# Performance work log

Hardware: AMD Instinct MI355X
Metric: run time of the kernel (lower is better)

Reference implementation:

```python
import jax, jax.numpy as jnp
import numpy as np

EPS = 1e-12  # torch f.normalize eps


def _rms_norm(x, g):
    # f.normalize(x, dim=1) * g * sqrt(C): L2-normalize over channel dim
    c = x.shape[1]
    n = jnp.maximum(jnp.linalg.norm(x, axis=1, keepdims=True), EPS)
    return x / n * g * (c ** 0.5)


def setup_inputs() -> dict:
    key = jax.random.key(0)
    ks = jax.random.split(key, 5)
    b, dim, H, W = 32, 256, 64, 64
    heads, dim_head, num_mem = 4, 32, 4
    hidden = heads * dim_head
    return {
        "x": jax.random.normal(ks[0], (b, dim, H, W), dtype=jnp.float32),
        "g1": jnp.ones((1, dim, 1, 1), dtype=jnp.float32),
        "mem_kv": jax.random.normal(ks[1], (2, heads, dim_head, num_mem), dtype=jnp.float32),
        "w_qkv": jax.random.normal(ks[2], (3 * hidden, dim), dtype=jnp.float32) * (1.0 / np.sqrt(dim)),
        "w_out": jax.random.normal(ks[3], (dim, hidden), dtype=jnp.float32) * (1.0 / np.sqrt(hidden)),
        "b_out": jnp.zeros((dim,), dtype=jnp.float32),
        "g2": jnp.ones((1, dim, 1, 1), dtype=jnp.float32),
    }


def reference(x, g1, mem_kv, w_qkv, w_out, b_out, g2):
    b, c, H, W = x.shape
    _, heads, dim_head, num_mem = mem_kv.shape
    n = H * W
    scale = dim_head ** -0.5

    xn = _rms_norm(x, g1)
    # 1x1 conv qkv projection: [b, 3*hidden, H, W]
    qkv = jnp.einsum('oc,bchw->bohw', w_qkv, xn)
    hidden = heads * dim_head
    q, k, v = jnp.split(qkv, 3, axis=1)
    # b (h d) x y -> b h d (x y)
    q = q.reshape(b, heads, dim_head, n)
    k = k.reshape(b, heads, dim_head, n)
    v = v.reshape(b, heads, dim_head, n)

    mk = jnp.broadcast_to(mem_kv[0], (b, heads, dim_head, num_mem))
    mv = jnp.broadcast_to(mem_kv[1], (b, heads, dim_head, num_mem))
    k = jnp.concatenate([mk, k], axis=-1)
    v = jnp.concatenate([mv, v], axis=-1)

    q = jax.nn.softmax(q, axis=-2) * scale  # softmax over head dim d
    k = jax.nn.softmax(k, axis=-1)          # softmax over sequence n

    context = jnp.einsum('bhdn,bhen->bhde', k, v)   # [b,h,d,e]
    out = jnp.einsum('bhde,bhdn->bhen', context, q)  # [b,h,e,n]
    out = out.reshape(b, hidden, H, W)

    o = jnp.einsum('oc,bchw->bohw', w_out, out) + b_out[None, :, None, None]
    return _rms_norm(o, g2)
```

## Files before the change

kernel.cpp:

```cpp
#include <hip/hip_runtime.h>
#include <math.h>

#define CC   256
#define HW   4096
#define OC3  384
#define HID  128
#define DH   32
#define NM   4
#define NPART 8
#define SCALE 0.17677669529663688f

typedef __bf16 bf16x8 __attribute__((ext_vector_type(8)));
typedef float  f32x4  __attribute__((ext_vector_type(4)));

__device__ __forceinline__ ushort f2bf(float x) {
    union { float f; unsigned u; } v; v.f = x;
    unsigned r = v.u + 0x7fffu + ((v.u >> 16) & 1u);
    return (ushort)(r >> 16);
}
__device__ __forceinline__ float bf2f(ushort b) {
    union { unsigned u; float f; } v; v.u = ((unsigned)b) << 16; return v.f;
}
__device__ __forceinline__ void g2l16(const void* g, void* l) {
    __builtin_amdgcn_global_load_lds(
        (const __attribute__((address_space(1))) void*)g,
        (__attribute__((address_space(3))) void*)l, 16, 0, 0);
}

__global__ void k_prep(const float* __restrict__ wqkv, const float* __restrict__ g1,
                       const float* __restrict__ wout,
                       ushort* __restrict__ wq2t, ushort* __restrict__ woutt) {
    int o = blockIdx.x, t = threadIdx.x;
    wq2t[(size_t)o * CC + t] = f2bf(wqkv[(size_t)o * CC + t] * g1[t] * 16.0f);
    if (o < CC && t < HID) woutt[(size_t)o * HID + t] = f2bf(wout[(size_t)o * HID + t]);
}

__global__ __launch_bounds__(256) void k_xn(const float* __restrict__ x,
                                            ushort* __restrict__ xnT) {
    __shared__ float xt[256 * 36];
    __shared__ float ps[8 * 33];
    __shared__ float invn[32];
    int tid = threadIdx.x;
    int pix0 = blockIdx.x * 32;
    int b = pix0 >> 12, hw0 = pix0 & 4095;
    int p = tid & 31, cg = tid >> 5;
    const float* xb = x + (size_t)b * CC * HW + hw0;
    {
        int cr = tid >> 3;
        int chunk = tid & 7;
        #pragma unroll
        for (int pass = 0; pass < 8; ++pass) {
            int c = pass * 32 + cr;
            float4 v = *(const float4*)&xb[(size_t)c * HW + chunk * 4];
            *(float4*)&xt[c * 36 + chunk * 4] = v;
        }
    }
    __syncthreads();
    float s = 0.f;
    #pragma unroll 8
    for (int i = 0; i < 32; ++i) { float v = xt[(cg * 32 + i) * 36 + p]; s += v * v; }
    ps[cg * 33 + p] = s;
    __syncthreads();
    if (tid < 32) {
        float t = 0.f;
        #pragma unroll
        for (int g = 0; g < 8; ++g) t += ps[g * 33 + tid];
        invn[tid] = 1.0f / fmaxf(sqrtf(t), 1e-12f);
    }
    __syncthreads();
    float inv = invn[p];
    ushort* dst = xnT + ((size_t)(pix0 + p)) * CC + cg * 32;
    #pragma unroll
    for (int q = 0; q < 4; ++q) {
        uint4 pk; ushort* o8 = (ushort*)&pk;
        #pragma unroll
        for (int i = 0; i < 8; ++i) o8[i] = f2bf(xt[(cg * 32 + q * 8 + i) * 36 + p] * inv);
        *(uint4*)&dst[q * 8] = pk;
    }
}

__global__ __launch_bounds__(256) void k_qkv(const ushort* __restrict__ wq2t,
        const ushort* __restrict__ xnT, ushort* __restrict__ qkv) {
    __shared__ ushort As[128 * 32];
    __shared__ ushort Bs[128 * 32];
    int tid = threadIdx.x;
    int lin = blockIdx.x + 3 * (blockIdx.y + 32 * blockIdx.z);
    int swz = (lin & 7) * 384 + (lin >> 3);
    int m0 = (swz % 3) * 128;
    int t_ = swz / 3;
    int p0 = (t_ & 31) * 128;
    int b  = t_ >> 5;
    int lane = tid & 63, wid = tid >> 6;
    int l15 = tid & 15, quad = (tid >> 4) & 3;
    int wm = wid >> 1, wn = wid & 1;
    int rsub = lane >> 2, csub = (lane & 3) * 8;
    const ushort* Ab = wq2t + (size_t)m0 * CC;
    const ushort* Bb = xnT + ((size_t)(b * HW + p0)) * CC;
    f32x4 acc[4][4];
    #pragma unroll
    for (int i = 0; i < 4; ++i)
        #pragma unroll
        for (int j = 0; j < 4; ++j) acc[i][j] = (f32x4){0.f, 0.f, 0.f, 0.f};
    for (int k0 = 0; k0 < CC; k0 += 32) {
        __syncthreads();
        #pragma unroll
        for (int q = 0; q < 2; ++q) {
            int rw = wid * 32 + q * 16;
            g2l16(Ab + (size_t)(rw + rsub) * CC + k0 + csub, &As[rw * 32]);
            g2l16(Bb + (size_t)(rw + rsub) * CC + k0 + csub, &Bs[rw * 32]);
        }
        __syncthreads();
        bf16x8 af[4], bfr[4];
        #pragma unroll
        for (int mt = 0; mt < 4; ++mt)
            af[mt] = *(const bf16x8*)&As[(wm * 64 + mt * 16 + l15) * 32 + quad * 8];
        #pragma unroll
        for (int nt = 0; nt < 4; ++nt)
            bfr[nt] = *(const bf16x8*)&Bs[(wn * 64 + nt * 16 + l15) * 32 + quad * 8];
        #pragma unroll
        for (int mt = 0; mt < 4; ++mt)
            #pragma unroll
            for (int nt = 0; nt < 4; ++nt)
                acc[mt][nt] = __builtin_amdgcn_mfma_f32_16x16x32_bf16(
                                  af[mt], bfr[nt], acc[mt][nt], 0, 0, 0);
    }
    #pragma unroll
    for (int mt = 0; mt < 4; ++mt) {
        int o = m0 + wm * 64 + mt * 16 + quad * 4;
        #pragma unroll
        for (int nt = 0; nt < 4; ++nt) {
            int pix = p0 + wn * 64 + nt * 16 + l15;
            ushort* dst = qkv + ((size_t)(b * OC3 + o)) * HW + pix;
            #pragma unroll
            for (int r = 0; r < 4; ++r) dst[(size_t)r * HW] = f2bf(acc[mt][nt][r]);
        }
    }
}

__global__ void k_ksoft(const ushort* __restrict__ qkv, const float* __restrict__ memkv,
                        float* __restrict__ kmaxb, float* __restrict__ rsumb) {
    int row = blockIdx.x * 4 + (threadIdx.x >> 6);
    int lane = threadIdx.x & 63;
    int b = row >> 7, hd = row & 127;
    const ushort* kp = qkv + ((size_t)(b * OC3 + HID + hd)) * HW;
    float m = -1e30f;
    #pragma unroll
    for (int i0 = 0; i0 < HW; i0 += 512) {
        uint4 pk = *(const uint4*)&kp[i0 + lane * 8];
        const ushort* e = (const ushort*)&pk;
        #pragma unroll
        for (int j = 0; j < 8; ++j) m = fmaxf(m, bf2f(e[j]));
    }
    #pragma unroll
    for (int s = 1; s < 64; s <<= 1) m = fmaxf(m, __shfl_xor(m, s));
    const float* mk = memkv + hd * NM;
    #pragma unroll
    for (int j = 0; j < NM; ++j) m = fmaxf(m, mk[j]);
    float s = 0.f;
    #pragma unroll
    for (int i0 = 0; i0 < HW; i0 += 512) {
        uint4 pk = *(const uint4*)&kp[i0 + lane * 8];
        const ushort* e = (const ushort*)&pk;
        #pragma unroll
        for (int j = 0; j < 8; ++j) s += __expf(bf2f(e[j]) - m);
    }
    #pragma unroll
    for (int t = 1; t < 64; t <<= 1) s += __shfl_xor(s, t);
    #pragma unroll
    for (int j = 0; j < NM; ++j) s += __expf(mk[j] - m);
    if (lane == 0) { kmaxb[row] = m; rsumb[row] = 1.0f / s; }
}

__global__ __launch_bounds__(256) void k_ctx(const ushort* __restrict__ qkv,
        const float* __restrict__ memkv, const float* __restrict__ kmaxb,
        const float* __restrict__ rsumb, float* __restrict__ ctxp) {
    __shared__ float kl[DH][65];
    __shared__ float vl[DH][65];
    __shared__ float red[256 * 33];
    int tid = threadIdx.x;
    int bh = blockIdx.x;
    int part = blockIdx.y;
    int b = bh >> 2, h = bh & 3;
    int lr = tid >> 3;
    int nn8 = (tid & 7) * 8;
    const ushort* kp = qkv + ((size_t)(b * OC3 + HID + h * DH) + lr) * HW + part * 512 + nn8;
    const ushort* vp = qkv + ((size_t)(b * OC3 + 2 * HID + h * DH) + lr) * HW + part * 512 + nn8;
    int rowbase = bh * DH;
    float kmr = kmaxb[rowbase + lr], rsr = rsumb[rowbase + lr];
    int slot = tid & 31, nng = tid >> 5;
    int d0 = (slot >> 2) * 4, e0 = (slot & 3) * 8;
    float acc[4][8];
    #pragma unroll
    for (int i = 0; i < 4; ++i)
        #pragma unroll
        for (int j = 0; j < 8; ++j) acc[i][j] = 0.f;
    for (int n0 = 0; n0 < 512; n0 += 64) {
        __syncthreads();
        uint4 kv4 = *(const uint4*)&kp[n0];
        uint4 vv4 = *(const uint4*)&vp[n0];
        const ushort* ke = (const ushort*)&kv4;
        const ushort* ve = (const ushort*)&vv4;
        #pragma unroll
        for (int j = 0; j < 8; ++j) {
            kl[lr][nn8 + j] = __expf(bf2f(ke[j]) - kmr) * rsr;
            vl[lr][nn8 + j] = bf2f(ve[j]);
        }
        __syncthreads();
        #pragma unroll 2
        for (int t = 0; t < 8; ++t) {
            int nn = nng * 8 + t;
            float kv[4], vv[8];
            #pragma unroll
            for (int i = 0; i < 4; ++i) kv[i] = kl[d0 + i][nn];
            #pragma unroll
            for (int j = 0; j < 8; ++j) vv[j] = vl[e0 + j][nn];
            #pragma unroll
            for (int i = 0; i < 4; ++i)
                #pragma unroll
                for (int j = 0; j < 8; ++j) acc[i][j] += kv[i] * vv[j];
        }
    }
    __syncthreads();
    #pragma unroll
    for (int i = 0; i < 4; ++i)
        #pragma unroll
        for (int j = 0; j < 8; ++j) red[tid * 33 + i * 8 + j] = acc[i][j];
    __syncthreads();
    #pragma unroll
    for (int q = 0; q < 4; ++q) {
        int o = tid * 4 + q;
        int d = o >> 5, e = o & 31;
        int sl = (d >> 2) * 4 + (e >> 3);
        int k = (d & 3) * 8 + (e & 7);
        float s = 0.f;
        #pragma unroll
        for (int g = 0; g < 8; ++g) s += red[(g * 32 + sl) * 33 + k];
        if (part == 0) {
            float km = kmaxb[rowbase + d], rsm = rsumb[rowbase + d];
            #pragma unroll
            for (int m = 0; m < NM; ++m) {
                float kw = __expf(memkv[(h * DH + d) * NM + m] - km) * rsm;
                s += kw * memkv[512 + (h * DH + e) * NM + m];
            }
        }
        ctxp[(size_t)part * 131072 + (size_t)bh * 1024 + o] = s;
    }
}

__global__ __launch_bounds__(256) void k_w2(const float* __restrict__ ctxp,
        const ushort* __restrict__ woutt, ushort* __restrict__ W2) {
    __shared__ ushort ctxb[4 * 32 * 40];
    int tid = threadIdx.x, b = blockIdx.x;
    int wid = tid >> 6;
    int l15 = tid & 15, quad = (tid >> 4) & 3;
    #pragma unroll
    for (int j = 0; j < 16; ++j) {
        int idx = tid + j * 256;
        float s = 0.f;
        #pragma unroll
        for (int p = 0; p < NPART; ++p)
            s += ctxp[(size_t)p * 131072 + (size_t)b * 4096 + idx];
        int h = idx >> 10, d = (idx >> 5) & 31, e = idx & 31;
        ctxb[(h * 32 + d) * 40 + e] = f2bf(s);
    }
    __syncthreads();
    #pragma unroll
    for (int h = 0; h < 4; ++h) {
        f32x4 acc[4][2];
        #pragma unroll
        for (int i = 0; i < 4; ++i)
            #pragma unroll
            for (int j = 0; j < 2; ++j) acc[i][j] = (f32x4){0.f, 0.f, 0.f, 0.f};
        bf16x8 af[4], bfr[2];
        #pragma unroll
        for (int mt = 0; mt < 4; ++mt)
            af[mt] = *(const bf16x8*)&woutt[(size_t)(wid * 64 + mt * 16 + l15) * HID
                                            + h * DH + quad * 8];
        #pragma unroll
        for (int nt = 0; nt < 2; ++nt)
            bfr[nt] = *(const bf16x8*)&ctxb[(h * 32 + nt * 16 + l15) * 40 + quad * 8];
        #pragma unroll
        for (int mt = 0; mt < 4; ++mt)
            #pragma unroll
            for (int nt = 0; nt < 2; ++nt)
                acc[mt][nt] = __builtin_amdgcn_mfma_f32_16x16x32_bf16(
                                  af[mt], bfr[nt], acc[mt][nt], 0, 0, 0);
        #pragma unroll
        for (int mt = 0; mt < 4; ++mt)
            #pragma unroll
            for (int nt = 0; nt < 2; ++nt)
                #pragma unroll
                for (int r = 0; r < 4; ++r) {
                    int oc = wid * 64 + mt * 16 + quad * 4 + r;
                    int d  = nt * 16 + l15;
                    W2[((size_t)b * CC + oc) * HID + h * DH + d] = f2bf(acc[mt][nt][r]);
                }
    }
}

__global__ __launch_bounds__(256) void k_final(const ushort* __restrict__ qkv,
        const ushort* __restrict__ W2, const float* __restrict__ bout,
        const float* __restrict__ g2, float* __restrict__ y) {
    __shared__ __align__(16) ushort sq[64 * 136];
    __shared__ __align__(16) ushort Ws[256 * 32];
    __shared__ float red[64 * 17];
    __shared__ float invs[64];
    __shared__ float bl[256];
    __shared__ float gl[256];
    int tid = threadIdx.x;
    int b = blockIdx.y;
    int hwb = blockIdx.x * 64;
    int lane = tid & 63, wid = tid >> 6;
    int l15 = tid & 15, quad = (tid >> 4) & 3;
    bl[tid] = bout[tid];
    gl[tid] = g2[tid];

    {
        const ushort* qp = qkv + ((size_t)b * OC3 + wid * DH) * HW + hwb + lane;
        float vd[32];
        float m = -1e30f;
        #pragma unroll
        for (int d = 0; d < 32; ++d) {
            float v = bf2f(qp[(size_t)d * HW]);
            vd[d] = v; m = fmaxf(m, v);
        }
        float s = 0.f;
        #pragma unroll
        for (int d = 0; d < 32; ++d) { float e = __expf(vd[d] - m); vd[d] = e; s += e; }
        float r_ = SCALE / s;
        #pragma unroll
        for (int q8 = 0; q8 < 4; ++q8) {
            uint4 pk; ushort* o8 = (ushort*)&pk;
            #pragma unroll
            for (int i = 0; i < 8; ++i) o8[i] = f2bf(vd[q8 * 8 + i] * r_);
            *(uint4*)&sq[lane * 136 + wid * DH + q8 * 8] = pk;
        }
    }

    f32x4 acc[4][4];
    #pragma unroll
    for (int i = 0; i < 4; ++i)
        #pragma unroll
        for (int j = 0; j < 4; ++j) acc[i][j] = (f32x4){0.f, 0.f, 0.f, 0.f};
    int rsub = lane >> 2, csub = (lane & 3) * 8;
    const ushort* W2b = W2 + (size_t)b * CC * HID;
    for (int k0 = 0; k0 < HID; k0 += 32) {
        __syncthreads();
        #pragma unroll
        for (int q = 0; q < 4; ++q) {
            int rw = wid * 64 + q * 16;
            g2l16(W2b + (size_t)(rw + rsub) * HID + k0 + csub, &Ws[rw * 32]);
        }
        __syncthreads();
        bf16x8 af[4], bfr[4];
        #pragma unroll
        for (int mt = 0; mt < 4; ++mt)
            af[mt] = *(const bf16x8*)&Ws[(wid * 64 + mt * 16 + l15) * 32 + quad * 8];
        #pragma unroll
        for (int nt = 0; nt < 4; ++nt)
            bfr[nt] = *(const bf16x8*)&sq[(nt * 16 + l15) * 136 + k0 + quad * 8];
        #pragma unroll
        for (int mt = 0; mt < 4; ++mt)
            #pragma unroll
            for (int nt = 0; nt < 4; ++nt)
                acc[mt][nt] = __builtin_amdgcn_mfma_f32_16x16x32_bf16(
                                  af[mt], bfr[nt], acc[mt][nt], 0, 0, 0);
    }

    float part[4] = {0.f, 0.f, 0.f, 0.f};
    #pragma unroll
    for (int mt = 0; mt < 4; ++mt)
        #pragma unroll
        for (int r = 0; r < 4; ++r) {
            int oc = wid * 64 + mt * 16 + quad * 4 + r;
            float bo = bl[oc];
            #pragma unroll
            for (int nt = 0; nt < 4; ++nt) {
                float v = acc[mt][nt][r] + bo;
                acc[mt][nt][r] = v;
                part[nt] += v * v;
            }
        }
    __syncthreads();
    #pragma unroll
    for (int nt = 0; nt < 4; ++nt)
        red[(nt * 16 + l15) * 17 + wid * 4 + quad] = part[nt];
    __syncthreads();
    if (tid < 64) {
        float s = 0.f;
        #pragma unroll
        for (int g = 0; g < 16; ++g) s += red[tid * 17 + g];
        invs[tid] = 1.0f / fmaxf(sqrtf(s), 1e-12f);
    }
    __syncthreads();
    #pragma unroll
    for (int mt = 0; mt < 4; ++mt)
        #pragma unroll
        for (int nt = 0; nt < 4; ++nt) {
            int pix = nt * 16 + l15;
            float iv = invs[pix];
            #pragma unroll
            for (int r = 0; r < 4; ++r) {
                int oc = wid * 64 + mt * 16 + quad * 4 + r;
                y[((size_t)(b * CC + oc)) * HW + hwb + pix] = acc[mt][nt][r] * iv * gl[oc] * 16.0f;
            }
        }
}

extern "C" void kernel_launch(void* const* d_in, const int* in_sizes, int n_in,
                              void* d_out, int out_size, void* d_ws, size_t ws_size,
                              hipStream_t stream) {
    const float* x     = (const float*)d_in[0];
    const float* g1    = (const float*)d_in[1];
    const float* memkv = (const float*)d_in[2];
    const float* wqkv  = (const float*)d_in[3];
    const float* wout  = (const float*)d_in[4];
    const float* bout  = (const float*)d_in[5];
    const float* g2    = (const float*)d_in[6];
    float* y = (float*)d_out;

    char* w = (char*)d_ws;
    ushort* wq2t  = (ushort*)w;  w += (size_t)OC3 * CC * 2;
    ushort* woutt = (ushort*)w;  w += (size_t)CC * HID * 2;
    float*  kmaxb = (float*)w;   w += 4096 * 4;
    float*  rsumb = (float*)w;   w += 4096 * 4;
    float*  ctxp  = (float*)w;   w += (size_t)NPART * 131072 * 4;
    ushort* W2    = (ushort*)w;  w += (size_t)32 * CC * HID * 2;
    ushort* xnT   = (ushort*)w;  w += (size_t)32 * HW * CC * 2;
    ushort* qkv   = (ushort*)w;  w += (size_t)32 * OC3 * HW * 2;

    k_prep  <<<dim3(384),       dim3(256), 0, stream>>>(wqkv, g1, wout, wq2t, woutt);
    k_xn    <<<dim3(4096),      dim3(256), 0, stream>>>(x, xnT);
    k_qkv   <<<dim3(3, 32, 32), dim3(256), 0, stream>>>(wq2t, xnT, qkv);
    k_ksoft <<<dim3(1024),      dim3(256), 0, stream>>>(qkv, memkv, kmaxb, rsumb);
    k_ctx   <<<dim3(128, 8),    dim3(256), 0, stream>>>(qkv, memkv, kmaxb, rsumb, ctxp);
    k_w2    <<<dim3(32),        dim3(256), 0, stream>>>(ctxp, woutt, W2);
    k_final <<<dim3(64, 32),    dim3(256), 0, stream>>>(qkv, W2, bout, g2, y);
}
```

Baseline: 368.9 us.

## Fuse input L2 normalization into QKV GEMM, applying inverse norm in epilogue

Removes the separate k_xn kernel and its bf16 transposed xnT intermediate. The QKV GEMM now loads raw fp32 x tiles, transposes and converts them to bf16 in shared memory, and accumulates per-pixel sum of squares along the way. The inverse norm is applied to the accumulator in the epilogue. Each of the three M-tile blocks re-reads fp32 x and redoes the conversion, and the un-normalized bf16 rounding changes precision slightly, in exchange for dropping a full write and read of xnT.

```diff
diff --git a/kernel.cpp b/kernel.cpp
--- a/kernel.cpp
+++ b/kernel.cpp
@@ -35,54 +35,13 @@
     if (o < CC && t < HID) woutt[(size_t)o * HID + t] = f2bf(wout[(size_t)o * HID + t]);
 }
 
-__global__ __launch_bounds__(256) void k_xn(const float* __restrict__ x,
-                                            ushort* __restrict__ xnT) {
-    __shared__ float xt[256 * 36];
-    __shared__ float ps[8 * 33];
-    __shared__ float invn[32];
-    int tid = threadIdx.x;
-    int pix0 = blockIdx.x * 32;
-    int b = pix0 >> 12, hw0 = pix0 & 4095;
-    int p = tid & 31, cg = tid >> 5;
-    const float* xb = x + (size_t)b * CC * HW + hw0;
-    {
-        int cr = tid >> 3;
-        int chunk = tid & 7;
-        #pragma unroll
-        for (int pass = 0; pass < 8; ++pass) {
-            int c = pass * 32 + cr;
-            float4 v = *(const float4*)&xb[(size_t)c * HW + chunk * 4];
-            *(float4*)&xt[c * 36 + chunk * 4] = v;
-        }
-    }
-    __syncthreads();
-    float s = 0.f;
-    #pragma unroll 8
-    for (int i = 0; i < 32; ++i) { float v = xt[(cg * 32 + i) * 36 + p]; s += v * v; }
-    ps[cg * 33 + p] = s;
-    __syncthreads();
-    if (tid < 32) {
-        float t = 0.f;
-        #pragma unroll
-        for (int g = 0; g < 8; ++g) t += ps[g * 33 + tid];
-        invn[tid] = 1.0f / fmaxf(sqrtf(t), 1e-12f);
-    }
-    __syncthreads();
-    float inv = invn[p];
-    ushort* dst = xnT + ((size_t)(pix0 + p)) * CC + cg * 32;
-    #pragma unroll
-    for (int q = 0; q < 4; ++q) {
-        uint4 pk; ushort* o8 = (ushort*)&pk;
-        #pragma unroll
-        for (int i = 0; i < 8; ++i) o8[i] = f2bf(xt[(cg * 32 + q * 8 + i) * 36 + p] * inv);
-        *(uint4*)&dst[q * 8] = pk;
-    }
-}
-
 __global__ __launch_bounds__(256) void k_qkv(const ushort* __restrict__ wq2t,
-        const ushort* __restrict__ xnT, ushort* __restrict__ qkv) {
-    __shared__ ushort As[128 * 32];
-    __shared__ ushort Bs[128 * 32];
+        const float* __restrict__ x, ushort* __restrict__ qkv) {
+    __shared__ __align__(16) ushort As[128 * 32];
+    __shared__ __align__(16) ushort Bs[128 * 40];
+    __shared__ __align__(16) float  xt[32 * 132];
+    __shared__ float nrm[256];
+    __shared__ float invp[128];
     int tid = threadIdx.x;
     int lin = blockIdx.x + 3 * (blockIdx.y + 32 * blockIdx.z);
     int swz = (lin & 7) * 384 + (lin >> 3);
@@ -94,8 +53,13 @@
     int l15 = tid & 15, quad = (tid >> 4) & 3;
     int wm = wid >> 1, wn = wid & 1;
     int rsub = lane >> 2, csub = (lane & 3) * 8;
+    int cb = tid >> 5;
+    int p4 = (tid & 31) * 4;
+    int tpix = tid & 127;
+    int tc8  = (tid >> 7) * 8;
     const ushort* Ab = wq2t + (size_t)m0 * CC;
-    const ushort* Bb = xnT + ((size_t)(b * HW + p0)) * CC;
+    const float*  xb = x + ((size_t)b * CC) * HW + p0;
+    float psum = 0.f;
     f32x4 acc[4][4];
     #pragma unroll
     for (int i = 0; i < 4; ++i)
@@ -107,7 +71,25 @@
         for (int q = 0; q < 2; ++q) {
             int rw = wid * 32 + q * 16;
             g2l16(Ab + (size_t)(rw + rsub) * CC + k0 + csub, &As[rw * 32]);
-            g2l16(Bb + (size_t)(rw + rsub) * CC + k0 + csub, &Bs[rw * 32]);
+        }
+        #pragma unroll
+        for (int rr = 0; rr < 4; ++rr) {
+            int c = rr * 8 + cb;
+            float4 v = *(const float4*)&xb[(size_t)(k0 + c) * HW + p4];
+            *(float4*)&xt[c * 132 + p4] = v;
+        }
+        __syncthreads();
+        #pragma unroll
+        for (int rr = 0; rr < 2; ++rr) {
+            int c8 = tc8 + rr * 16;
+            uint4 pk; ushort* o8 = (ushort*)&pk;
+            #pragma unroll
+            for (int i = 0; i < 8; ++i) {
+                float v = xt[(c8 + i) * 132 + tpix];
+                psum += v * v;
+                o8[i] = f2bf(v);
+            }
+            *(uint4*)&Bs[tpix * 40 + c8] = pk;
         }
         __syncthreads();
         bf16x8 af[4], bfr[4];
@@ -116,7 +98,7 @@
             af[mt] = *(const bf16x8*)&As[(wm * 64 + mt * 16 + l15) * 32 + quad * 8];
         #pragma unroll
         for (int nt = 0; nt < 4; ++nt)
-            bfr[nt] = *(const bf16x8*)&Bs[(wn * 64 + nt * 16 + l15) * 32 + quad * 8];
+            bfr[nt] = *(const bf16x8*)&Bs[(wn * 64 + nt * 16 + l15) * 40 + quad * 8];
         #pragma unroll
         for (int mt = 0; mt < 4; ++mt)
             #pragma unroll
@@ -124,15 +106,23 @@
                 acc[mt][nt] = __builtin_amdgcn_mfma_f32_16x16x32_bf16(
                                   af[mt], bfr[nt], acc[mt][nt], 0, 0, 0);
     }
+    nrm[tid] = psum;
+    __syncthreads();
+    if (tid < 128) {
+        float s = nrm[tid] + nrm[tid + 128];
+        invp[tid] = 1.0f / fmaxf(sqrtf(s), 1e-12f);
+    }
+    __syncthreads();
     #pragma unroll
     for (int mt = 0; mt < 4; ++mt) {
         int o = m0 + wm * 64 + mt * 16 + quad * 4;
         #pragma unroll
         for (int nt = 0; nt < 4; ++nt) {
-            int pix = p0 + wn * 64 + nt * 16 + l15;
-            ushort* dst = qkv + ((size_t)(b * OC3 + o)) * HW + pix;
-            #pragma unroll
-            for (int r = 0; r < 4; ++r) dst[(size_t)r * HW] = f2bf(acc[mt][nt][r]);
+            int pixl = wn * 64 + nt * 16 + l15;
+            float iv = invp[pixl];
+            ushort* dst = qkv + ((size_t)(b * OC3 + o)) * HW + p0 + pixl;
+            #pragma unroll
+            for (int r = 0; r < 4; ++r) dst[(size_t)r * HW] = f2bf(acc[mt][nt][r] * iv);
         }
     }
 }
@@ -426,12 +416,10 @@
     float*  rsumb = (float*)w;   w += 4096 * 4;
     float*  ctxp  = (float*)w;   w += (size_t)NPART * 131072 * 4;
     ushort* W2    = (ushort*)w;  w += (size_t)32 * CC * HID * 2;
-    ushort* xnT   = (ushort*)w;  w += (size_t)32 * HW * CC * 2;
     ushort* qkv   = (ushort*)w;  w += (size_t)32 * OC3 * HW * 2;
 
     k_prep  <<<dim3(384),       dim3(256), 0, stream>>>(wqkv, g1, wout, wq2t, woutt);
-    k_xn    <<<dim3(4096),      dim3(256), 0, stream>>>(x, xnT);
-    k_qkv   <<<dim3(3, 32, 32), dim3(256), 0, stream>>>(wq2t, xnT, qkv);
+    k_qkv   <<<dim3(3, 32, 32), dim3(256), 0, stream>>>(wq2t, x, qkv);
     k_ksoft <<<dim3(1024),      dim3(256), 0, stream>>>(qkv, memkv, kmaxb, rsumb);
     k_ctx   <<<dim3(128, 8),    dim3(256), 0, stream>>>(qkv, memkv, kmaxb, rsumb, ctxp);
     k_w2    <<<dim3(32),        dim3(256), 0, stream>>>(ctxp, woutt, W2);
```

After: 358.2 us. -2.9%, faster.

## Double-buffer LDS tiles and XOR-swizzle columns in QKV GEMM

Applied to the files above, without the earlier changes.

The QKV projection GEMM now keeps two LDS buffers, so the next K-slice loads from global memory while MFMAs run on the current one. This removes one barrier per iteration. The 16-byte column chunks are also XOR-swizzled by row to cut LDS bank conflicts on fragment reads. In exchange the kernel uses twice the LDS, which may lower occupancy, and correctness depends on global_load_lds completing before the single trailing barrier.

```diff
diff --git a/kernel.cpp b/kernel.cpp
--- a/kernel.cpp
+++ b/kernel.cpp
@@ -81,8 +81,8 @@
 
 __global__ __launch_bounds__(256) void k_qkv(const ushort* __restrict__ wq2t,
         const ushort* __restrict__ xnT, ushort* __restrict__ qkv) {
-    __shared__ ushort As[128 * 32];
-    __shared__ ushort Bs[128 * 32];
+    __shared__ __align__(16) ushort As[2][128 * 32];
+    __shared__ __align__(16) ushort Bs[2][128 * 32];
     int tid = threadIdx.x;
     int lin = blockIdx.x + 3 * (blockIdx.y + 32 * blockIdx.z);
     int swz = (lin & 7) * 384 + (lin >> 3);
@@ -93,7 +93,7 @@
     int lane = tid & 63, wid = tid >> 6;
     int l15 = tid & 15, quad = (tid >> 4) & 3;
     int wm = wid >> 1, wn = wid & 1;
-    int rsub = lane >> 2, csub = (lane & 3) * 8;
+    int rsub = lane >> 2;
     const ushort* Ab = wq2t + (size_t)m0 * CC;
     const ushort* Bb = xnT + ((size_t)(b * HW + p0)) * CC;
     f32x4 acc[4][4];
@@ -101,28 +101,42 @@
     for (int i = 0; i < 4; ++i)
         #pragma unroll
         for (int j = 0; j < 4; ++j) acc[i][j] = (f32x4){0.f, 0.f, 0.f, 0.f};
-    for (int k0 = 0; k0 < CC; k0 += 32) {
-        __syncthreads();
+
+    auto stage = [&](int buf, int k0) {
         #pragma unroll
         for (int q = 0; q < 2; ++q) {
             int rw = wid * 32 + q * 16;
-            g2l16(Ab + (size_t)(rw + rsub) * CC + k0 + csub, &As[rw * 32]);
-            g2l16(Bb + (size_t)(rw + rsub) * CC + k0 + csub, &Bs[rw * 32]);
-        }
-        __syncthreads();
+            int r  = rw + rsub;
+            int sc = (lane & 3) ^ ((r >> 1) & 3);
+            g2l16(Ab + (size_t)r * CC + k0 + sc * 8, &As[buf][rw * 32]);
+            g2l16(Bb + (size_t)r * CC + k0 + sc * 8, &Bs[buf][rw * 32]);
+        }
+    };
+
+    stage(0, 0);
+    __syncthreads();
+    #pragma unroll
+    for (int s = 0; s < 8; ++s) {
+        int cur = s & 1;
+        if (s < 7) stage(cur ^ 1, (s + 1) * 32);
         bf16x8 af[4], bfr[4];
         #pragma unroll
-        for (int mt = 0; mt < 4; ++mt)
-            af[mt] = *(const bf16x8*)&As[(wm * 64 + mt * 16 + l15) * 32 + quad * 8];
-        #pragma unroll
-        for (int nt = 0; nt < 4; ++nt)
-            bfr[nt] = *(const bf16x8*)&Bs[(wn * 64 + nt * 16 + l15) * 32 + quad * 8];
+        for (int mt = 0; mt < 4; ++mt) {
+            int ra = wm * 64 + mt * 16 + l15;
+            af[mt] = *(const bf16x8*)&As[cur][ra * 32 + ((quad ^ ((ra >> 1) & 3)) << 3)];
+        }
+        #pragma unroll
+        for (int nt = 0; nt < 4; ++nt) {
+            int rb = wn * 64 + nt * 16 + l15;
+            bfr[nt] = *(const bf16x8*)&Bs[cur][rb * 32 + ((quad ^ ((rb >> 1) & 3)) << 3)];
+        }
         #pragma unroll
         for (int mt = 0; mt < 4; ++mt)
             #pragma unroll
             for (int nt = 0; nt < 4; ++nt)
                 acc[mt][nt] = __builtin_amdgcn_mfma_f32_16x16x32_bf16(
                                   af[mt], bfr[nt], acc[mt][nt], 0, 0, 0);
+        __syncthreads();
     }
     #pragma unroll
     for (int mt = 0; mt < 4; ++mt) {
```

Result: no change. 376.1 us (+2.0%).
